# Optimization experiments

Hardware: AMD Instinct MI355X
Metric: run time of the kernel (lower is better)

The kernel has to match this reference:

```python
import jax, jax.numpy as jnp
import numpy as np

INPUT, UNITS, MOTOR, OUT = 1, 256, 64, 32
REM = UNITS - MOTOR
COMMAND = max(int(0.4 * REM), 1)   # 76
INTER = REM - COMMAND              # 116
B, L = 512, 1024
DIMS = [(INPUT, INTER), (INTER, COMMAND), (COMMAND, MOTOR)]


def setup_inputs() -> dict:
    rng = np.random.default_rng(0)
    inp = {}
    inp['dt'] = jnp.asarray(rng.random((B, L, INPUT)).astype(np.float32))
    inp['hx'] = jnp.asarray(rng.standard_normal((B, UNITS)).astype(np.float32))
    for i, (din, h) in enumerate(DIMS):
        c = din + h
        s = 1.0 / np.sqrt(c)
        for nm in ('W1', 'W2', 'Wa', 'Wb'):
            inp[f'l{i}_{nm}'] = jnp.asarray((rng.standard_normal((h, c)) * s).astype(np.float32))
        for nm in ('b1', 'b2', 'ba', 'bb'):
            inp[f'l{i}_{nm}'] = jnp.asarray((rng.standard_normal((h,)) * s).astype(np.float32))
        # NCP sparsity mask: random cross-layer connectivity (density ~0.5), dense recurrent block
        cross = (rng.random((h, din)) < 0.5).astype(np.int32)
        rec = np.ones((h, h), dtype=np.int32)
        inp[f'mask{i}'] = jnp.asarray(np.concatenate([cross, rec], axis=1))
    so = 1.0 / np.sqrt(MOTOR)
    inp['Wout'] = jnp.asarray((rng.standard_normal((OUT, MOTOR)) * so).astype(np.float32))
    inp['bout'] = jnp.asarray((rng.standard_normal((OUT,)) * so).astype(np.float32))
    return inp


def _cfc_cell(x, W1, W2, Wa, Wb, b1, b2, ba, bb, mask):
    # CfC 'default' mode, ts = 1.0 (CfC called without timespans; dt is the input signal)
    m = mask.astype(x.dtype)
    ff1 = jnp.tanh(x @ (W1 * m).T + b1)
    ff2 = jnp.tanh(x @ (W2 * m).T + b2)
    t_interp = jax.nn.sigmoid((x @ Wa.T + ba) + (x @ Wb.T + bb))
    return ff1 * (1.0 - t_interp) + t_interp * ff2


def _forward(dt, hx, params, masks, Wout, bout):
    # hx layout follows WiredCfCCell layer order: [inter, command, motor]
    h0, h1, h2 = jnp.split(hx, [INTER, INTER + COMMAND], axis=1)

    def step(carry, dt_t):
        h0, h1, h2 = carry
        h0 = _cfc_cell(jnp.concatenate([dt_t, h0], axis=-1), *params[0], masks[0])
        h1 = _cfc_cell(jnp.concatenate([h0, h1], axis=-1), *params[1], masks[1])
        h2 = _cfc_cell(jnp.concatenate([h1, h2], axis=-1), *params[2], masks[2])
        return (h0, h1, h2), h2

    _, ys = jax.lax.scan(step, (h0, h1, h2), jnp.swapaxes(dt, 0, 1))  # (L, B, MOTOR)
    readout = jnp.swapaxes(ys, 0, 1)  # (B, L, MOTOR)
    return readout @ Wout.T + bout    # (B, L, OUT)


def reference(dt, hx, l0_W1, l0_W2, l0_Wa, l0_Wb, l0_b1, l0_b2, l0_ba, l0_bb, l1_W1, l1_W2, l1_Wa, l1_Wb, l1_b1, l1_b2, l1_ba, l1_bb, l2_W1, l2_W2, l2_Wa, l2_Wb, l2_b1, l2_b2, l2_ba, l2_bb, mask0, mask1, mask2, Wout, bout):
    params = [
        (l0_W1, l0_W2, l0_Wa, l0_Wb, l0_b1, l0_b2, l0_ba, l0_bb),
        (l1_W1, l1_W2, l1_Wa, l1_Wb, l1_b1, l1_b2, l1_ba, l1_bb),
        (l2_W1, l2_W2, l2_Wa, l2_Wb, l2_b1, l2_b2, l2_ba, l2_bb),
    ]
    return _forward(dt, hx, params, (mask0, mask1, mask2), Wout, bout)
```

## Files before the change

kernel.cpp:

```cpp
#include <hip/hip_runtime.h>
#include <stdint.h>

typedef _Float16 f16;
typedef _Float16 h2v __attribute__((ext_vector_type(2)));
typedef _Float16 F16x8 __attribute__((ext_vector_type(8)));
typedef float F32x4 __attribute__((ext_vector_type(4)));

#define MFMA16(a,b,c) __builtin_amdgcn_mfma_f32_16x16x32_f16((a),(b),(c),0,0,0)
#define S12f 2.8853900817779268f
#define SABf (-1.4426950408889634f)

static __device__ __forceinline__ float exp2f_b(float x){ return __builtin_amdgcn_exp2f(x); }

static __device__ __forceinline__ f16 cfc_act(F32x4 a){
  float E1=exp2f_b(a[0]), E2=exp2f_b(a[1]), es=exp2f_b(a[2]+a[3]);
  float t1=E1+1.f, u=(E2+1.f)*(1.f+es);
  float num=u-(E2-E1);
  float r=__builtin_amdgcn_rcpf(t1*u);
  return (f16)(1.f-2.f*num*r);
}
static __device__ __forceinline__ int fidx(int k,int b){ return ((k>>3)<<7)+(b<<3)+(k&7); }

static __device__ __forceinline__ void tick_barrier(){
  asm volatile("s_waitcnt lgkmcnt(0)" ::: "memory");
  __builtin_amdgcn_s_barrier();
}

__global__ __launch_bounds__(256) void cfc_prep(
    const float* __restrict__ W10,const float* __restrict__ W20,const float* __restrict__ Wa0,const float* __restrict__ Wb0,
    const float* __restrict__ b10,const float* __restrict__ b20,const float* __restrict__ ba0,const float* __restrict__ bb0,
    const int* __restrict__ M0,
    const float* __restrict__ W11,const float* __restrict__ W21,const float* __restrict__ Wa1,const float* __restrict__ Wb1,
    const float* __restrict__ b11,const float* __restrict__ b21,const float* __restrict__ ba1,const float* __restrict__ bb1,
    const int* __restrict__ M1,
    const float* __restrict__ W12,const float* __restrict__ W22,const float* __restrict__ Wa2,const float* __restrict__ Wb2,
    const float* __restrict__ b12,const float* __restrict__ b22,const float* __restrict__ ba2,const float* __restrict__ bb2,
    const int* __restrict__ M2,
    const float* __restrict__ Wo, f16* __restrict__ ws)
{
  int idx=blockIdx.x*256+threadIdx.x;
  if(idx>=21312) return;
  int tile=idx>>6, lane=idx&63, ml=lane&15, grp=lane>>4;
  F16x8 fr;
  if(tile<329){
    int rt,kt,c,lay;
    const float *w1,*w2,*wa,*wb,*c1,*c2,*ca,*cb; const int* M;
    if(tile<116){ rt=tile>>2; kt=tile&3; c=117; lay=0;
      w1=W10;w2=W20;wa=Wa0;wb=Wb0;M=M0;c1=b10;c2=b20;ca=ba0;cb=bb0; }
    else if(tile<249){ int u=tile-116; rt=u/7; kt=u-rt*7; c=192; lay=1;
      w1=W11;w2=W21;wa=Wa1;wb=Wb1;M=M1;c1=b11;c2=b21;ca=ba1;cb=bb1; }
    else { int u=tile-249; rt=u/5; kt=u-rt*5; c=140; lay=2;
      w1=W12;w2=W22;wa=Wa2;wb=Wb2;M=M2;c1=b12;c2=b22;ca=ba2;cb=bb2; }
    int n=rt*4+(ml>>2), mat=ml&3;
    const float* W =(mat==0)?w1:(mat==1)?w2:(mat==2)?wa:wb;
    const float* Bv=(mat==0)?c1:(mat==1)?c2:(mat==2)?ca:cb;
    float sc=(mat<2)?S12f:SABf;
    int k0=kt*32+grp*8;
    #pragma unroll
    for(int j=0;j<8;++j){
      int k=k0+j; float v=0.f; int col=-1;
      if(lay==0){       if(k<116) col=1+k; else if(k==124) col=0; else if(k==125) col=-2; }
      else if(lay==1){  if(k<116) col=k; else if(k>=128 && k<204) col=116+(k-128); else if(k==125) col=-2; }
      else {            if(k<76) col=k; else if(k>=96 && k<160) col=76+(k-96); else if(k==88) col=-2; }
      if(col>=0){ v=W[n*c+col]; if(mat<2) v*=(float)M[n*c+col]; }
      else if(col==-2){ v=Bv[n]; }
      fr[j]=(f16)(v*sc);
    }
  } else {
    int u=tile-329, rt=u>>1, kt=u&1;
    int o=rt*16+ml, k0=kt*32+grp*8;
    #pragma unroll
    for(int j=0;j<8;++j) fr[j]=(f16)Wo[o*64+k0+j];
  }
  ((F16x8*)ws)[idx]=fr;
}

__global__ __launch_bounds__(1024,4) void cfc_main(
    const float* __restrict__ dtp, const float* __restrict__ hxp,
    const f16* __restrict__ ws, float* __restrict__ outp)
{
  const int tid=threadIdx.x, lane=tid&63, w=tid>>6;
  const int b_l=lane&15, g_l=lane>>4;
  const int gb0=blockIdx.x*16;

  __shared__ alignas(16) f16 H0[2][2048];
  __shared__ alignas(16) f16 H1[2][1536];
  __shared__ alignas(16) f16 H2[2][1024];
  __shared__ f16 DTS[16448];

  const F16x8* wsf=(const F16x8*)ws;
  F32x4 ZED; ZED[0]=0.f; ZED[1]=0.f; ZED[2]=0.f; ZED[3]=0.f;

  for(int i=tid;i<4096;i+=1024) ((f16*)H0)[i]=(f16)0.f;
  for(int i=tid;i<3072;i+=1024) ((f16*)H1)[i]=(f16)0.f;
  for(int i=tid;i<2048;i+=1024) ((f16*)H2)[i]=(f16)0.f;
  for(int i=tid;i<16448;i+=1024){
    int t=i>>4, b=i&15;
    DTS[i]=(t<1024)?(f16)dtp[(size_t)(gb0+b)*1024+t]:(f16)0.f;
  }
  __syncthreads();
  for(int i=tid;i<4096;i+=1024){ int b=i>>8,u=i&255; f16 v=(f16)hxp[(size_t)(gb0+b)*256+u];
    if(u<116){ H0[0][fidx(u,b)]=v; H0[1][fidx(u,b)]=v; }
    else if(u<192){ int n=u-116; H1[0][fidx(n,b)]=v; H1[1][fidx(n,b)]=v; }
    else { int n=u-192; H2[0][fidx(n,b)]=v; H2[1][fidx(n,b)]=v; }
  }
  if(tid<16){
    H0[1][fidx(124,tid)]=DTS[tid];
    H0[0][fidx(125,tid)]=(f16)1.f; H0[1][fidx(125,tid)]=(f16)1.f;
    H1[0][fidx(88,tid)]=(f16)1.f;  H1[1][fidx(88,tid)]=(f16)1.f;
  }
  __syncthreads();

  if(w<2){
    F16x8 w1f[2][7], w0f[2][4];
    #pragma unroll
    for(int j=0;j<2;++j){ int rt=2*w+j;
      #pragma unroll
      for(int kt=0;kt<7;++kt) w1f[j][kt]=wsf[(116+rt*7+kt)*64+lane]; }
    #pragma unroll
    for(int m=0;m<2;++m){ int rt=2*w+m;
      #pragma unroll
      for(int kt=0;kt<4;++kt) w0f[m][kt]=wsf[(rt*4+kt)*64+lane]; }
    const int wb1a=fidx((2*w+0)*4+g_l,b_l), wb1b=fidx((2*w+1)*4+g_l,b_l);
    const int wb0a=fidx((2*w+0)*4+g_l,b_l), wb0b=fidx((2*w+1)*4+g_l,b_l);
#define MIXED_TICK(I_,P_) do{ \
      if((I_)<=1024){ \
        F16x8 Af0=((const F16x8*)H0[(P_)^1])[0*64+lane]; \
        F16x8 Af1=((const F16x8*)H0[(P_)^1])[1*64+lane]; \
        F16x8 Af2=((const F16x8*)H0[(P_)^1])[2*64+lane]; \
        F16x8 Af3=((const F16x8*)H0[(P_)^1])[3*64+lane]; \
        F32x4 a1_0=MFMA16(w1f[0][0],Af0,ZED), a1_1=MFMA16(w1f[1][0],Af0,ZED); \
        F32x4 a0_0=MFMA16(w0f[0][0],Af0,ZED), a0_1=MFMA16(w0f[1][0],Af0,ZED); \
        a1_0=MFMA16(w1f[0][1],Af1,a1_0); a1_1=MFMA16(w1f[1][1],Af1,a1_1); \
        a0_0=MFMA16(w0f[0][1],Af1,a0_0); a0_1=MFMA16(w0f[1][1],Af1,a0_1); \
        a1_0=MFMA16(w1f[0][2],Af2,a1_0); a1_1=MFMA16(w1f[1][2],Af2,a1_1); \
        a0_0=MFMA16(w0f[0][2],Af2,a0_0); a0_1=MFMA16(w0f[1][2],Af2,a0_1); \
        a1_0=MFMA16(w1f[0][3],Af3,a1_0); a1_1=MFMA16(w1f[1][3],Af3,a1_1); \
        a0_0=MFMA16(w0f[0][3],Af3,a0_0); a0_1=MFMA16(w0f[1][3],Af3,a0_1); \
        _Pragma("unroll") \
        for(int kt=0;kt<3;++kt){ \
          F16x8 Hf=((const F16x8*)H1[(P_)^1])[kt*64+lane]; \
          a1_0=MFMA16(w1f[0][4+kt],Hf,a1_0); a1_1=MFMA16(w1f[1][4+kt],Hf,a1_1); \
        } \
        if((I_)>=1){ H1[P_][wb1a]=cfc_act(a1_0); H1[P_][wb1b]=cfc_act(a1_1); } \
        if((I_)<=1023){ H0[P_][wb0a]=cfc_act(a0_0); H0[P_][wb0b]=cfc_act(a0_1); } \
      } }while(0)
    for(int I2=0;I2<1028;I2+=2){
      MIXED_TICK(I2,0);   tick_barrier();
      MIXED_TICK(I2+1,1); tick_barrier();
    }
#undef MIXED_TICK
  } else if(w<7){
    F16x8 wf[3][7];
    #pragma unroll
    for(int j=0;j<3;++j){ int rt=4+3*(w-2)+j;
      #pragma unroll
      for(int kt=0;kt<7;++kt) wf[j][kt]=wsf[(116+rt*7+kt)*64+lane]; }
    const int wb0=fidx((4+3*(w-2)+0)*4+g_l,b_l);
    const int wb1=fidx((4+3*(w-2)+1)*4+g_l,b_l);
    const int wb2=fidx((4+3*(w-2)+2)*4+g_l,b_l);
#define L1_TICK(I_,P_) do{ \
      if((I_)>=1 && (I_)<=1024){ \
        F16x8 Af0=((const F16x8*)H0[(P_)^1])[0*64+lane]; \
        F16x8 Af1=((const F16x8*)H0[(P_)^1])[1*64+lane]; \
        F16x8 Af2=((const F16x8*)H0[(P_)^1])[2*64+lane]; \
        F16x8 Af3=((const F16x8*)H0[(P_)^1])[3*64+lane]; \
        F32x4 a0=MFMA16(wf[0][0],Af0,ZED), a1=MFMA16(wf[1][0],Af0,ZED), a2=MFMA16(wf[2][0],Af0,ZED); \
        a0=MFMA16(wf[0][1],Af1,a0); a1=MFMA16(wf[1][1],Af1,a1); a2=MFMA16(wf[2][1],Af1,a2); \
        a0=MFMA16(wf[0][2],Af2,a0); a1=MFMA16(wf[1][2],Af2,a1); a2=MFMA16(wf[2][2],Af2,a2); \
        a0=MFMA16(wf[0][3],Af3,a0); a1=MFMA16(wf[1][3],Af3,a1); a2=MFMA16(wf[2][3],Af3,a2); \
        _Pragma("unroll") \
        for(int kt=0;kt<3;++kt){ \
          F16x8 Hf=((const F16x8*)H1[(P_)^1])[kt*64+lane]; \
          a0=MFMA16(wf[0][4+kt],Hf,a0); a1=MFMA16(wf[1][4+kt],Hf,a1); a2=MFMA16(wf[2][4+kt],Hf,a2); \
        } \
        H1[P_][wb0]=cfc_act(a0); H1[P_][wb1]=cfc_act(a1); H1[P_][wb2]=cfc_act(a2); \
      } }while(0)
    for(int I2=0;I2<1028;I2+=2){
      L1_TICK(I2,0);   tick_barrier();
      L1_TICK(I2+1,1); tick_barrier();
    }
#undef L1_TICK
  } else if(w<12){
    F16x8 wf[5][4];
    #pragma unroll
    for(int m=0;m<5;++m){ int rt=4+5*(w-7)+m;
      #pragma unroll
      for(int kt=0;kt<4;++kt) wf[m][kt]=wsf[(rt*4+kt)*64+lane]; }
    int wbx[5];
    #pragma unroll
    for(int m=0;m<5;++m) wbx[m]=fidx((4+5*(w-7)+m)*4+g_l,b_l);
    const bool dost=(w<9);
    const int q=lane&7, bb=(lane>>3)+8*(w-7);
    char* outPtr=(char*)outp + ((size_t)(gb0+bb)*1024)*128 + q*16;
#define L0_TICK(I_,P_) do{ \
      if((I_)<=1023){ \
        F16x8 Af0=((const F16x8*)H0[(P_)^1])[0*64+lane]; \
        F16x8 Af1=((const F16x8*)H0[(P_)^1])[1*64+lane]; \
        F16x8 Af2=((const F16x8*)H0[(P_)^1])[2*64+lane]; \
        F16x8 Af3=((const F16x8*)H0[(P_)^1])[3*64+lane]; \
        F32x4 a0=MFMA16(wf[0][0],Af0,ZED), a1=MFMA16(wf[1][0],Af0,ZED); \
        F32x4 a2=MFMA16(wf[2][0],Af0,ZED), a3=MFMA16(wf[3][0],Af0,ZED); \
        F32x4 a4=MFMA16(wf[4][0],Af0,ZED); \
        a0=MFMA16(wf[0][1],Af1,a0); a1=MFMA16(wf[1][1],Af1,a1); \
        a2=MFMA16(wf[2][1],Af1,a2); a3=MFMA16(wf[3][1],Af1,a3); \
        a4=MFMA16(wf[4][1],Af1,a4); \
        a0=MFMA16(wf[0][2],Af2,a0); a1=MFMA16(wf[1][2],Af2,a1); \
        a2=MFMA16(wf[2][2],Af2,a2); a3=MFMA16(wf[3][2],Af2,a3); \
        a4=MFMA16(wf[4][2],Af2,a4); \
        a0=MFMA16(wf[0][3],Af3,a0); a1=MFMA16(wf[1][3],Af3,a1); \
        a2=MFMA16(wf[2][3],Af3,a2); a3=MFMA16(wf[3][3],Af3,a3); \
        a4=MFMA16(wf[4][3],Af3,a4); \
        H0[P_][wbx[0]]=cfc_act(a0); H0[P_][wbx[1]]=cfc_act(a1); \
        H0[P_][wbx[2]]=cfc_act(a2); H0[P_][wbx[3]]=cfc_act(a3); \
        H0[P_][wbx[4]]=cfc_act(a4); \
      } \
      if(dost && (I_)>=3 && (I_)<=1026){ \
        F16x8 v=((const F16x8*)H2[(P_)^1])[q*16+bb]; \
        *(F16x8*)outPtr=v; outPtr+=128; \
      } }while(0)
    for(int I2=0;I2<1028;I2+=2){
      L0_TICK(I2,0);   tick_barrier();
      L0_TICK(I2+1,1); tick_barrier();
    }
#undef L0_TICK
  } else {
    F16x8 wc[4][5];
    #pragma unroll
    for(int j=0;j<4;++j){ int rt=4*(w-12)+j;
      #pragma unroll
      for(int kt=0;kt<5;++kt) wc[j][kt]=wsf[(249+rt*5+kt)*64+lane]; }
    int wbx[4];
    #pragma unroll
    for(int j=0;j<4;++j) wbx[j]=fidx((4*(w-12)+j)*4+g_l,b_l);
    const bool dodt=(w==15);
#define L2_TICK(I_,P_) do{ \
      if(dodt && lane<16 && (I_)<=1022) H0[P_][fidx(124,lane)]=DTS[((I_)+1)*16+lane]; \
      if((I_)>=2 && (I_)<=1025){ \
        F16x8 Cf0=((const F16x8*)H1[(P_)^1])[0*64+lane]; \
        F16x8 Cf1=((const F16x8*)H1[(P_)^1])[1*64+lane]; \
        F16x8 Cf2=((const F16x8*)H1[(P_)^1])[2*64+lane]; \
        F16x8 Cf3=((const F16x8*)H2[(P_)^1])[0*64+lane]; \
        F16x8 Cf4=((const F16x8*)H2[(P_)^1])[1*64+lane]; \
        F32x4 a0=MFMA16(wc[0][0],Cf0,ZED), a1=MFMA16(wc[1][0],Cf0,ZED); \
        F32x4 a2=MFMA16(wc[2][0],Cf0,ZED), a3=MFMA16(wc[3][0],Cf0,ZED); \
        a0=MFMA16(wc[0][1],Cf1,a0); a1=MFMA16(wc[1][1],Cf1,a1); \
        a2=MFMA16(wc[2][1],Cf1,a2); a3=MFMA16(wc[3][1],Cf1,a3); \
        a0=MFMA16(wc[0][2],Cf2,a0); a1=MFMA16(wc[1][2],Cf2,a1); \
        a2=MFMA16(wc[2][2],Cf2,a2); a3=MFMA16(wc[3][2],Cf2,a3); \
        a0=MFMA16(wc[0][3],Cf3,a0); a1=MFMA16(wc[1][3],Cf3,a1); \
        a2=MFMA16(wc[2][3],Cf3,a2); a3=MFMA16(wc[3][3],Cf3,a3); \
        a0=MFMA16(wc[0][4],Cf4,a0); a1=MFMA16(wc[1][4],Cf4,a1); \
        a2=MFMA16(wc[2][4],Cf4,a2); a3=MFMA16(wc[3][4],Cf4,a3); \
        H2[P_][wbx[0]]=cfc_act(a0); H2[P_][wbx[1]]=cfc_act(a1); \
        H2[P_][wbx[2]]=cfc_act(a2); H2[P_][wbx[3]]=cfc_act(a3); \
      } }while(0)
    for(int I2=0;I2<1028;I2+=2){
      L2_TICK(I2,0);   tick_barrier();
      L2_TICK(I2+1,1); tick_barrier();
    }
#undef L2_TICK
  }
}

__global__ __launch_bounds__(256) void cfc_ro(
    const float* __restrict__ Wo, const float* __restrict__ bo, float* __restrict__ outp)
{
  __shared__ h2v wT[1024];
  __shared__ float bs[32];
  int tid=threadIdx.x;
  for(int i=tid;i<1024;i+=256){ int kp=i>>5,o=i&31;
    h2v v; v[0]=(f16)Wo[o*64+2*kp]; v[1]=(f16)Wo[o*64+2*kp+1]; wT[i]=v; }
  if(tid<32) bs[tid]=bo[tid];
  __syncthreads();
  size_t s=(size_t)blockIdx.x*256+tid;
  float* slot=outp+s*32;
  h2v x[32];
  #pragma unroll
  for(int r=0;r<8;++r) ((F16x8*)x)[r]=((const F16x8*)slot)[r];
  float y[32];
  #pragma unroll
  for(int o=0;o<32;++o){
    float acc=bs[o];
    #pragma unroll
    for(int kp=0;kp<32;++kp) acc=__builtin_amdgcn_fdot2(x[kp],wT[kp*32+o],acc,false);
    y[o]=acc;
  }
  #pragma unroll
  for(int r=0;r<8;++r) ((float4*)slot)[r]=((const float4*)y)[r];
}

extern "C" void kernel_launch(void* const* d_in, const int* in_sizes, int n_in,
                              void* d_out, int out_size, void* d_ws, size_t ws_size,
                              hipStream_t stream)
{
  (void)in_sizes; (void)n_in; (void)out_size; (void)ws_size;
  f16* ws=(f16*)d_ws;
  cfc_prep<<<84,256,0,stream>>>(
    (const float*)d_in[2],(const float*)d_in[3],(const float*)d_in[4],(const float*)d_in[5],
    (const float*)d_in[6],(const float*)d_in[7],(const float*)d_in[8],(const float*)d_in[9],
    (const int*)d_in[10],
    (const float*)d_in[11],(const float*)d_in[12],(const float*)d_in[13],(const float*)d_in[14],
    (const float*)d_in[15],(const float*)d_in[16],(const float*)d_in[17],(const float*)d_in[18],
    (const int*)d_in[19],
    (const float*)d_in[20],(const float*)d_in[21],(const float*)d_in[22],(const float*)d_in[23],
    (const float*)d_in[24],(const float*)d_in[25],(const float*)d_in[26],(const float*)d_in[27],
    (const int*)d_in[28],
    (const float*)d_in[29], ws);
  cfc_main<<<32,1024,0,stream>>>(
    (const float*)d_in[0],(const float*)d_in[1], ws, (float*)d_out);
  cfc_ro<<<2048,256,0,stream>>>(
    (const float*)d_in[29],(const float*)d_in[30],(float*)d_out);
}
```

Before: 1.067 ms.

## Merge Wa/Wb gate matrices and regroup weight tiles by matrix type

Before the MFMA, the Wa and Wb gate weights are summed in prep, since the reference only uses their sum. This drops from four matrices per output row to three and cuts MFMA work per tick by about a quarter. The tile layout changes so that each 16-row MFMA tile holds one matrix for 16 output units. The activation then combines three accumulators element-wise and writes 4 f16 values in one vector store. Waves are reassigned to the new tile counts with a remapped wave-to-task table, and one wave handles leftover layer-0 and layer-2 tiles together.

Measured after the change: 1.040 ms. -2.5%, faster.

```diff
diff --git a/kernel.cpp b/kernel.cpp
--- a/kernel.cpp
+++ b/kernel.cpp
@@ -3,6 +3,7 @@
 
 typedef _Float16 f16;
 typedef _Float16 h2v __attribute__((ext_vector_type(2)));
+typedef _Float16 F16x4 __attribute__((ext_vector_type(4)));
 typedef _Float16 F16x8 __attribute__((ext_vector_type(8)));
 typedef float F32x4 __attribute__((ext_vector_type(4)));
 
@@ -12,8 +13,8 @@
 
 static __device__ __forceinline__ float exp2f_b(float x){ return __builtin_amdgcn_exp2f(x); }
 
-static __device__ __forceinline__ f16 cfc_act(F32x4 a){
-  float E1=exp2f_b(a[0]), E2=exp2f_b(a[1]), es=exp2f_b(a[2]+a[3]);
+static __device__ __forceinline__ f16 cfc_act3(float p1,float p2,float ps){
+  float E1=exp2f_b(p1), E2=exp2f_b(p2), es=exp2f_b(ps);
   float t1=E1+1.f, u=(E2+1.f)*(1.f+es);
   float num=u-(E2-E1);
   float r=__builtin_amdgcn_rcpf(t1*u);
@@ -39,38 +40,36 @@
     const float* __restrict__ Wo, f16* __restrict__ ws)
 {
   int idx=blockIdx.x*256+threadIdx.x;
-  if(idx>=21312) return;
+  if(idx>=16704) return;
   int tile=idx>>6, lane=idx&63, ml=lane&15, grp=lane>>4;
+  int lay,nb,m,kt,c,h;
+  const float *w1,*w2,*wa,*wb,*c1,*c2,*ca,*cb; const int* M;
+  if(tile<96){ lay=0; int u=tile; kt=u&3; int q=u>>2; m=q%3; nb=q/3; c=117; h=116;
+    w1=W10;w2=W20;wa=Wa0;wb=Wb0;M=M0;c1=b10;c2=b20;ca=ba0;cb=bb0; }
+  else if(tile<201){ lay=1; int u=tile-96; kt=u%7; int q=u/7; m=q%3; nb=q/3; c=192; h=76;
+    w1=W11;w2=W21;wa=Wa1;wb=Wb1;M=M1;c1=b11;c2=b21;ca=ba1;cb=bb1; }
+  else { lay=2; int u=tile-201; kt=u%5; int q=u/5; m=q%3; nb=q/3; c=140; h=64;
+    w1=W12;w2=W22;wa=Wa2;wb=Wb2;M=M2;c1=b12;c2=b22;ca=ba2;cb=bb2; }
+  int n=nb*16+ml;
+  float sc=(m<2)?S12f:SABf;
+  int k0=kt*32+grp*8;
   F16x8 fr;
-  if(tile<329){
-    int rt,kt,c,lay;
-    const float *w1,*w2,*wa,*wb,*c1,*c2,*ca,*cb; const int* M;
-    if(tile<116){ rt=tile>>2; kt=tile&3; c=117; lay=0;
-      w1=W10;w2=W20;wa=Wa0;wb=Wb0;M=M0;c1=b10;c2=b20;ca=ba0;cb=bb0; }
-    else if(tile<249){ int u=tile-116; rt=u/7; kt=u-rt*7; c=192; lay=1;
-      w1=W11;w2=W21;wa=Wa1;wb=Wb1;M=M1;c1=b11;c2=b21;ca=ba1;cb=bb1; }
-    else { int u=tile-249; rt=u/5; kt=u-rt*5; c=140; lay=2;
-      w1=W12;w2=W22;wa=Wa2;wb=Wb2;M=M2;c1=b12;c2=b22;ca=ba2;cb=bb2; }
-    int n=rt*4+(ml>>2), mat=ml&3;
-    const float* W =(mat==0)?w1:(mat==1)?w2:(mat==2)?wa:wb;
-    const float* Bv=(mat==0)?c1:(mat==1)?c2:(mat==2)?ca:cb;
-    float sc=(mat<2)?S12f:SABf;
-    int k0=kt*32+grp*8;
-    #pragma unroll
-    for(int j=0;j<8;++j){
-      int k=k0+j; float v=0.f; int col=-1;
-      if(lay==0){       if(k<116) col=1+k; else if(k==124) col=0; else if(k==125) col=-2; }
-      else if(lay==1){  if(k<116) col=k; else if(k>=128 && k<204) col=116+(k-128); else if(k==125) col=-2; }
-      else {            if(k<76) col=k; else if(k>=96 && k<160) col=76+(k-96); else if(k==88) col=-2; }
-      if(col>=0){ v=W[n*c+col]; if(mat<2) v*=(float)M[n*c+col]; }
-      else if(col==-2){ v=Bv[n]; }
-      fr[j]=(f16)(v*sc);
-    }
-  } else {
-    int u=tile-329, rt=u>>1, kt=u&1;
-    int o=rt*16+ml, k0=kt*32+grp*8;
-    #pragma unroll
-    for(int j=0;j<8;++j) fr[j]=(f16)Wo[o*64+k0+j];
+  #pragma unroll
+  for(int j=0;j<8;++j){
+    int k=k0+j; float v=0.f; int col=-1;
+    if(lay==0){       if(k<116) col=1+k; else if(k==124) col=0; else if(k==125) col=-2; }
+    else if(lay==1){  if(k<116) col=k; else if(k>=128 && k<204) col=116+(k-128); else if(k==125) col=-2; }
+    else {            if(k<76) col=k; else if(k>=96 && k<160) col=76+(k-96); else if(k==88) col=-2; }
+    if(n<h){
+      if(col>=0){
+        if(m==0){ v=w1[n*c+col]*(float)M[n*c+col]; }
+        else if(m==1){ v=w2[n*c+col]*(float)M[n*c+col]; }
+        else { v=wa[n*c+col]+wb[n*c+col]; }
+      } else if(col==-2){
+        v=(m==0)?c1[n]:(m==1)?c2[n]:(ca[n]+cb[n]);
+      }
+    }
+    fr[j]=(f16)(v*sc);
   }
   ((F16x8*)ws)[idx]=fr;
 }
@@ -111,56 +110,104 @@
   }
   __syncthreads();
 
-  if(w<2){
-    F16x8 w1f[2][7], w0f[2][4];
-    #pragma unroll
-    for(int j=0;j<2;++j){ int rt=2*w+j;
-      #pragma unroll
-      for(int kt=0;kt<7;++kt) w1f[j][kt]=wsf[(116+rt*7+kt)*64+lane]; }
-    #pragma unroll
-    for(int m=0;m<2;++m){ int rt=2*w+m;
-      #pragma unroll
-      for(int kt=0;kt<4;++kt) w0f[m][kt]=wsf[(rt*4+kt)*64+lane]; }
-    const int wb1a=fidx((2*w+0)*4+g_l,b_l), wb1b=fidx((2*w+1)*4+g_l,b_l);
-    const int wb0a=fidx((2*w+0)*4+g_l,b_l), wb0b=fidx((2*w+1)*4+g_l,b_l);
-#define MIXED_TICK(I_,P_) do{ \
-      if((I_)<=1024){ \
+  int type, nb=0;
+  if(w==0){ type=0; }
+  else if(w==1){type=1;nb=0;} else if(w==5){type=1;nb=1;} else if(w==2){type=1;nb=2;}
+  else if(w==3){type=1;nb=3;} else if(w==7){type=1;nb=4;}
+  else if(w==4){type=3;nb=0;} else if(w==6){type=3;nb=1;} else if(w==10){type=3;nb=2;}
+  else { type=2; nb=(w==8)?0:(w==12)?1:(w==9)?2:(w==13)?3:(w==14)?4:(w==11)?5:6; }
+
+  if(type==0){
+    F16x8 wm0[3][4], wm2[3][5];
+    #pragma unroll
+    for(int m=0;m<3;++m){
+      #pragma unroll
+      for(int kt=0;kt<4;++kt) wm0[m][kt]=wsf[((7*3+m)*4+kt)*64+lane];
+      #pragma unroll
+      for(int kt=0;kt<5;++kt) wm2[m][kt]=wsf[(201+(3*3+m)*5+kt)*64+lane];
+    }
+    const int wk0=fidx(112+g_l*4,b_l);
+    const int wk2=fidx(48+g_l*4,b_l);
+#define MG_TICK(I_,P_) do{ \
+      if((I_)<=1023){ \
         F16x8 Af0=((const F16x8*)H0[(P_)^1])[0*64+lane]; \
         F16x8 Af1=((const F16x8*)H0[(P_)^1])[1*64+lane]; \
         F16x8 Af2=((const F16x8*)H0[(P_)^1])[2*64+lane]; \
         F16x8 Af3=((const F16x8*)H0[(P_)^1])[3*64+lane]; \
-        F32x4 a1_0=MFMA16(w1f[0][0],Af0,ZED), a1_1=MFMA16(w1f[1][0],Af0,ZED); \
-        F32x4 a0_0=MFMA16(w0f[0][0],Af0,ZED), a0_1=MFMA16(w0f[1][0],Af0,ZED); \
-        a1_0=MFMA16(w1f[0][1],Af1,a1_0); a1_1=MFMA16(w1f[1][1],Af1,a1_1); \
-        a0_0=MFMA16(w0f[0][1],Af1,a0_0); a0_1=MFMA16(w0f[1][1],Af1,a0_1); \
-        a1_0=MFMA16(w1f[0][2],Af2,a1_0); a1_1=MFMA16(w1f[1][2],Af2,a1_1); \
-        a0_0=MFMA16(w0f[0][2],Af2,a0_0); a0_1=MFMA16(w0f[1][2],Af2,a0_1); \
-        a1_0=MFMA16(w1f[0][3],Af3,a1_0); a1_1=MFMA16(w1f[1][3],Af3,a1_1); \
-        a0_0=MFMA16(w0f[0][3],Af3,a0_0); a0_1=MFMA16(w0f[1][3],Af3,a0_1); \
-        _Pragma("unroll") \
-        for(int kt=0;kt<3;++kt){ \
-          F16x8 Hf=((const F16x8*)H1[(P_)^1])[kt*64+lane]; \
-          a1_0=MFMA16(w1f[0][4+kt],Hf,a1_0); a1_1=MFMA16(w1f[1][4+kt],Hf,a1_1); \
-        } \
-        if((I_)>=1){ H1[P_][wb1a]=cfc_act(a1_0); H1[P_][wb1b]=cfc_act(a1_1); } \
-        if((I_)<=1023){ H0[P_][wb0a]=cfc_act(a0_0); H0[P_][wb0b]=cfc_act(a0_1); } \
+        F32x4 a0=MFMA16(wm0[0][0],Af0,ZED), a1=MFMA16(wm0[1][0],Af0,ZED), a2=MFMA16(wm0[2][0],Af0,ZED); \
+        a0=MFMA16(wm0[0][1],Af1,a0); a1=MFMA16(wm0[1][1],Af1,a1); a2=MFMA16(wm0[2][1],Af1,a2); \
+        a0=MFMA16(wm0[0][2],Af2,a0); a1=MFMA16(wm0[1][2],Af2,a1); a2=MFMA16(wm0[2][2],Af2,a2); \
+        a0=MFMA16(wm0[0][3],Af3,a0); a1=MFMA16(wm0[1][3],Af3,a1); a2=MFMA16(wm0[2][3],Af3,a2); \
+        if(g_l==0){ \
+          F16x4 v; v[0]=cfc_act3(a0[0],a1[0],a2[0]); v[1]=cfc_act3(a0[1],a1[1],a2[1]); \
+          v[2]=cfc_act3(a0[2],a1[2],a2[2]); v[3]=cfc_act3(a0[3],a1[3],a2[3]); \
+          *(F16x4*)&H0[P_][wk0]=v; } \
+      } \
+      if((I_)>=2 && (I_)<=1025){ \
+        F16x8 Cf0=((const F16x8*)H1[(P_)^1])[0*64+lane]; \
+        F16x8 Cf1=((const F16x8*)H1[(P_)^1])[1*64+lane]; \
+        F16x8 Cf2=((const F16x8*)H1[(P_)^1])[2*64+lane]; \
+        F16x8 Cf3=((const F16x8*)H2[(P_)^1])[0*64+lane]; \
+        F16x8 Cf4=((const F16x8*)H2[(P_)^1])[1*64+lane]; \
+        F32x4 c0=MFMA16(wm2[0][0],Cf0,ZED), c1=MFMA16(wm2[1][0],Cf0,ZED), c2=MFMA16(wm2[2][0],Cf0,ZED); \
+        c0=MFMA16(wm2[0][1],Cf1,c0); c1=MFMA16(wm2[1][1],Cf1,c1); c2=MFMA16(wm2[2][1],Cf1,c2); \
+        c0=MFMA16(wm2[0][2],Cf2,c0); c1=MFMA16(wm2[1][2],Cf2,c1); c2=MFMA16(wm2[2][2],Cf2,c2); \
+        c0=MFMA16(wm2[0][3],Cf3,c0); c1=MFMA16(wm2[1][3],Cf3,c1); c2=MFMA16(wm2[2][3],Cf3,c2); \
+        c0=MFMA16(wm2[0][4],Cf4,c0); c1=MFMA16(wm2[1][4],Cf4,c1); c2=MFMA16(wm2[2][4],Cf4,c2); \
+        F16x4 v; v[0]=cfc_act3(c0[0],c1[0],c2[0]); v[1]=cfc_act3(c0[1],c1[1],c2[1]); \
+        v[2]=cfc_act3(c0[2],c1[2],c2[2]); v[3]=cfc_act3(c0[3],c1[3],c2[3]); \
+        *(F16x4*)&H2[P_][wk2]=v; \
       } }while(0)
     for(int I2=0;I2<1028;I2+=2){
-      MIXED_TICK(I2,0);   tick_barrier();
-      MIXED_TICK(I2+1,1); tick_barrier();
-    }
-#undef MIXED_TICK
-  } else if(w<7){
+      MG_TICK(I2,0);   tick_barrier();
+      MG_TICK(I2+1,1); tick_barrier();
+    }
+#undef MG_TICK
+  } else if(type==1){
     F16x8 wf[3][7];
     #pragma unroll
-    for(int j=0;j<3;++j){ int rt=4+3*(w-2)+j;
-      #pragma unroll
-      for(int kt=0;kt<7;++kt) wf[j][kt]=wsf[(116+rt*7+kt)*64+lane]; }
-    const int wb0=fidx((4+3*(w-2)+0)*4+g_l,b_l);
-    const int wb1=fidx((4+3*(w-2)+1)*4+g_l,b_l);
-    const int wb2=fidx((4+3*(w-2)+2)*4+g_l,b_l);
+    for(int m=0;m<3;++m)
+      #pragma unroll
+      for(int kt=0;kt<7;++kt) wf[m][kt]=wsf[(96+(nb*3+m)*7+kt)*64+lane];
+    const int wk=fidx(nb*16+g_l*4,b_l);
+    const bool wr_ok=(nb<4)||(g_l<3);
 #define L1_TICK(I_,P_) do{ \
       if((I_)>=1 && (I_)<=1024){ \
+        F16x8 Af0=((const F16x8*)H0[(P_)^1])[0*64+lane]; \
+        F16x8 Af1=((const F16x8*)H0[(P_)^1])[1*64+lane]; \
+        F16x8 Af2=((const F16x8*)H0[(P_)^1])[2*64+lane]; \
+        F16x8 Af3=((const F16x8*)H0[(P_)^1])[3*64+lane]; \
+        F16x8 Hf0=((const F16x8*)H1[(P_)^1])[0*64+lane]; \
+        F16x8 Hf1=((const F16x8*)H1[(P_)^1])[1*64+lane]; \
+        F16x8 Hf2=((const F16x8*)H1[(P_)^1])[2*64+lane]; \
+        F32x4 a0=MFMA16(wf[0][0],Af0,ZED), a1=MFMA16(wf[1][0],Af0,ZED), a2=MFMA16(wf[2][0],Af0,ZED); \
+        a0=MFMA16(wf[0][1],Af1,a0); a1=MFMA16(wf[1][1],Af1,a1); a2=MFMA16(wf[2][1],Af1,a2); \
+        a0=MFMA16(wf[0][2],Af2,a0); a1=MFMA16(wf[1][2],Af2,a1); a2=MFMA16(wf[2][2],Af2,a2); \
+        a0=MFMA16(wf[0][3],Af3,a0); a1=MFMA16(wf[1][3],Af3,a1); a2=MFMA16(wf[2][3],Af3,a2); \
+        a0=MFMA16(wf[0][4],Hf0,a0); a1=MFMA16(wf[1][4],Hf0,a1); a2=MFMA16(wf[2][4],Hf0,a2); \
+        a0=MFMA16(wf[0][5],Hf1,a0); a1=MFMA16(wf[1][5],Hf1,a1); a2=MFMA16(wf[2][5],Hf1,a2); \
+        a0=MFMA16(wf[0][6],Hf2,a0); a1=MFMA16(wf[1][6],Hf2,a1); a2=MFMA16(wf[2][6],Hf2,a2); \
+        F16x4 v; v[0]=cfc_act3(a0[0],a1[0],a2[0]); v[1]=cfc_act3(a0[1],a1[1],a2[1]); \
+        v[2]=cfc_act3(a0[2],a1[2],a2[2]); v[3]=cfc_act3(a0[3],a1[3],a2[3]); \
+        if(wr_ok) *(F16x4*)&H1[P_][wk]=v; \
+      } }while(0)
+    for(int I2=0;I2<1028;I2+=2){
+      L1_TICK(I2,0);   tick_barrier();
+      L1_TICK(I2+1,1); tick_barrier();
+    }
+#undef L1_TICK
+  } else if(type==2){
+    F16x8 wf[3][4];
+    #pragma unroll
+    for(int m=0;m<3;++m)
+      #pragma unroll
+      for(int kt=0;kt<4;++kt) wf[m][kt]=wsf[((nb*3+m)*4+kt)*64+lane];
+    const int wk=fidx(nb*16+g_l*4,b_l);
+    const bool dost=(w==9)||(w==14);
+    const int q=lane&7, bb=(lane>>3)+8*((w==9)?0:1);
+    char* outPtr=(char*)outp + ((size_t)(gb0+bb)*1024)*128 + q*16;
+#define L0_TICK(I_,P_) do{ \
+      if((I_)<=1023){ \
         F16x8 Af0=((const F16x8*)H0[(P_)^1])[0*64+lane]; \
         F16x8 Af1=((const F16x8*)H0[(P_)^1])[1*64+lane]; \
         F16x8 Af2=((const F16x8*)H0[(P_)^1])[2*64+lane]; \
@@ -169,55 +216,13 @@
         a0=MFMA16(wf[0][1],Af1,a0); a1=MFMA16(wf[1][1],Af1,a1); a2=MFMA16(wf[2][1],Af1,a2); \
         a0=MFMA16(wf[0][2],Af2,a0); a1=MFMA16(wf[1][2],Af2,a1); a2=MFMA16(wf[2][2],Af2,a2); \
         a0=MFMA16(wf[0][3],Af3,a0); a1=MFMA16(wf[1][3],Af3,a1); a2=MFMA16(wf[2][3],Af3,a2); \
-        _Pragma("unroll") \
-        for(int kt=0;kt<3;++kt){ \
-          F16x8 Hf=((const F16x8*)H1[(P_)^1])[kt*64+lane]; \
-          a0=MFMA16(wf[0][4+kt],Hf,a0); a1=MFMA16(wf[1][4+kt],Hf,a1); a2=MFMA16(wf[2][4+kt],Hf,a2); \
-        } \
-        H1[P_][wb0]=cfc_act(a0); H1[P_][wb1]=cfc_act(a1); H1[P_][wb2]=cfc_act(a2); \
-      } }while(0)
-    for(int I2=0;I2<1028;I2+=2){
-      L1_TICK(I2,0);   tick_barrier();
-      L1_TICK(I2+1,1); tick_barrier();
-    }
-#undef L1_TICK
-  } else if(w<12){
-    F16x8 wf[5][4];
-    #pragma unroll
-    for(int m=0;m<5;++m){ int rt=4+5*(w-7)+m;
-      #pragma unroll
-      for(int kt=0;kt<4;++kt) wf[m][kt]=wsf[(rt*4+kt)*64+lane]; }
-    int wbx[5];
-    #pragma unroll
-    for(int m=0;m<5;++m) wbx[m]=fidx((4+5*(w-7)+m)*4+g_l,b_l);
-    const bool dost=(w<9);
-    const int q=lane&7, bb=(lane>>3)+8*(w-7);
-    char* outPtr=(char*)outp + ((size_t)(gb0+bb)*1024)*128 + q*16;
-#define L0_TICK(I_,P_) do{ \
-      if((I_)<=1023){ \
-        F16x8 Af0=((const F16x8*)H0[(P_)^1])[0*64+lane]; \
-        F16x8 Af1=((const F16x8*)H0[(P_)^1])[1*64+lane]; \
-        F16x8 Af2=((const F16x8*)H0[(P_)^1])[2*64+lane]; \
-        F16x8 Af3=((const F16x8*)H0[(P_)^1])[3*64+lane]; \
-        F32x4 a0=MFMA16(wf[0][0],Af0,ZED), a1=MFMA16(wf[1][0],Af0,ZED); \
-        F32x4 a2=MFMA16(wf[2][0],Af0,ZED), a3=MFMA16(wf[3][0],Af0,ZED); \
-        F32x4 a4=MFMA16(wf[4][0],Af0,ZED); \
-        a0=MFMA16(wf[0][1],Af1,a0); a1=MFMA16(wf[1][1],Af1,a1); \
-        a2=MFMA16(wf[2][1],Af1,a2); a3=MFMA16(wf[3][1],Af1,a3); \
-        a4=MFMA16(wf[4][1],Af1,a4); \
-        a0=MFMA16(wf[0][2],Af2,a0); a1=MFMA16(wf[1][2],Af2,a1); \
-        a2=MFMA16(wf[2][2],Af2,a2); a3=MFMA16(wf[3][2],Af2,a3); \
-        a4=MFMA16(wf[4][2],Af2,a4); \
-        a0=MFMA16(wf[0][3],Af3,a0); a1=MFMA16(wf[1][3],Af3,a1); \
-        a2=MFMA16(wf[2][3],Af3,a2); a3=MFMA16(wf[3][3],Af3,a3); \
-        a4=MFMA16(wf[4][3],Af3,a4); \
-        H0[P_][wbx[0]]=cfc_act(a0); H0[P_][wbx[1]]=cfc_act(a1); \
-        H0[P_][wbx[2]]=cfc_act(a2); H0[P_][wbx[3]]=cfc_act(a3); \
-        H0[P_][wbx[4]]=cfc_act(a4); \
+        F16x4 v; v[0]=cfc_act3(a0[0],a1[0],a2[0]); v[1]=cfc_act3(a0[1],a1[1],a2[1]); \
+        v[2]=cfc_act3(a0[2],a1[2],a2[2]); v[3]=cfc_act3(a0[3],a1[3],a2[3]); \
+        *(F16x4*)&H0[P_][wk]=v; \
       } \
       if(dost && (I_)>=3 && (I_)<=1026){ \
-        F16x8 v=((const F16x8*)H2[(P_)^1])[q*16+bb]; \
-        *(F16x8*)outPtr=v; outPtr+=128; \
+        F16x8 sv=((const F16x8*)H2[(P_)^1])[q*16+bb]; \
+        *(F16x8*)outPtr=sv; outPtr+=128; \
       } }while(0)
     for(int I2=0;I2<1028;I2+=2){
       L0_TICK(I2,0);   tick_barrier();
@@ -225,15 +230,13 @@
     }
 #undef L0_TICK
   } else {
-    F16x8 wc[4][5];
-    #pragma unroll
-    for(int j=0;j<4;++j){ int rt=4*(w-12)+j;
-      #pragma unroll
-      for(int kt=0;kt<5;++kt) wc[j][kt]=wsf[(249+rt*5+kt)*64+lane]; }
-    int wbx[4];
-    #pragma unroll
-    for(int j=0;j<4;++j) wbx[j]=fidx((4*(w-12)+j)*4+g_l,b_l);
-    const bool dodt=(w==15);
+    F16x8 wf[3][5];
+    #pragma unroll
+    for(int m=0;m<3;++m)
+      #pragma unroll
+      for(int kt=0;kt<5;++kt) wf[m][kt]=wsf[(201+(nb*3+m)*5+kt)*64+lane];
+    const int wk=fidx(nb*16+g_l*4,b_l);
+    const bool dodt=(w==6);
 #define L2_TICK(I_,P_) do{ \
       if(dodt && lane<16 && (I_)<=1022) H0[P_][fidx(124,lane)]=DTS[((I_)+1)*16+lane]; \
       if((I_)>=2 && (I_)<=1025){ \
@@ -242,18 +245,14 @@
         F16x8 Cf2=((const F16x8*)H1[(P_)^1])[2*64+lane]; \
         F16x8 Cf3=((const F16x8*)H2[(P_)^1])[0*64+lane]; \
         F16x8 Cf4=((const F16x8*)H2[(P_)^1])[1*64+lane]; \
-        F32x4 a0=MFMA16(wc[0][0],Cf0,ZED), a1=MFMA16(wc[1][0],Cf0,ZED); \
-        F32x4 a2=MFMA16(wc[2][0],Cf0,ZED), a3=MFMA16(wc[3][0],Cf0,ZED); \
-        a0=MFMA16(wc[0][1],Cf1,a0); a1=MFMA16(wc[1][1],Cf1,a1); \
-        a2=MFMA16(wc[2][1],Cf1,a2); a3=MFMA16(wc[3][1],Cf1,a3); \
-        a0=MFMA16(wc[0][2],Cf2,a0); a1=MFMA16(wc[1][2],Cf2,a1); \
-        a2=MFMA16(wc[2][2],Cf2,a2); a3=MFMA16(wc[3][2],Cf2,a3); \
-        a0=MFMA16(wc[0][3],Cf3,a0); a1=MFMA16(wc[1][3],Cf3,a1); \
-        a2=MFMA16(wc[2][3],Cf3,a2); a3=MFMA16(wc[3][3],Cf3,a3); \
-        a0=MFMA16(wc[0][4],Cf4,a0); a1=MFMA16(wc[1][4],Cf4,a1); \
-        a2=MFMA16(wc[2][4],Cf4,a2); a3=MFMA16(wc[3][4],Cf4,a3); \
-        H2[P_][wbx[0]]=cfc_act(a0); H2[P_][wbx[1]]=cfc_act(a1); \
-        H2[P_][wbx[2]]=cfc_act(a2); H2[P_][wbx[3]]=cfc_act(a3); \
+        F32x4 a0=MFMA16(wf[0][0],Cf0,ZED), a1=MFMA16(wf[1][0],Cf0,ZED), a2=MFMA16(wf[2][0],Cf0,ZED); \
+        a0=MFMA16(wf[0][1],Cf1,a0); a1=MFMA16(wf[1][1],Cf1,a1); a2=MFMA16(wf[2][1],Cf1,a2); \
+        a0=MFMA16(wf[0][2],Cf2,a0); a1=MFMA16(wf[1][2],Cf2,a1); a2=MFMA16(wf[2][2],Cf2,a2); \
+        a0=MFMA16(wf[0][3],Cf3,a0); a1=MFMA16(wf[1][3],Cf3,a1); a2=MFMA16(wf[2][3],Cf3,a2); \
+        a0=MFMA16(wf[0][4],Cf4,a0); a1=MFMA16(wf[1][4],Cf4,a1); a2=MFMA16(wf[2][4],Cf4,a2); \
+        F16x4 v; v[0]=cfc_act3(a0[0],a1[0],a2[0]); v[1]=cfc_act3(a0[1],a1[1],a2[1]); \
+        v[2]=cfc_act3(a0[2],a1[2],a2[2]); v[3]=cfc_act3(a0[3],a1[3],a2[3]); \
+        *(F16x4*)&H2[P_][wk]=v; \
       } }while(0)
     for(int I2=0;I2<1028;I2+=2){
       L2_TICK(I2,0);   tick_barrier();
@@ -296,7 +295,7 @@
 {
   (void)in_sizes; (void)n_in; (void)out_size; (void)ws_size;
   f16* ws=(f16*)d_ws;
-  cfc_prep<<<84,256,0,stream>>>(
+  cfc_prep<<<66,256,0,stream>>>(
     (const float*)d_in[2],(const float*)d_in[3],(const float*)d_in[4],(const float*)d_in[5],
     (const float*)d_in[6],(const float*)d_in[7],(const float*)d_in[8],(const float*)d_in[9],
     (const int*)d_in[10],
```
